# Kernel tuning notes

Measured on AMD Instinct MI355X. Metric: run time of the kernel, lower is better.

## Reference

```python
import jax, jax.numpy as jnp
import numpy as np

N_ATOMS = 50000
N_EDGES = 1_600_000
N_MOL = 500
HIDDEN = 128
FILTERS = 128
GAUSS = 50
LAYERS = 3
CUTOFF = 10.0
LOG2 = 0.6931471805599453


def ssp(x):
    # ShiftedSoftplus: softplus(x) - log(2)
    return jax.nn.softplus(x) - LOG2


def setup_inputs() -> dict:
    key = jax.random.key(0)
    ks = jax.random.split(key, 24)
    z = jax.random.randint(ks[0], (N_ATOMS,), 0, 100)
    pos = jax.random.uniform(ks[1], (N_ATOMS, 3), jnp.float32) * 5.0  # box keeps d < cutoff
    batch = jnp.sort(jax.random.randint(ks[2], (N_ATOMS,), 0, N_MOL))
    row = jax.random.randint(ks[3], (N_EDGES,), 0, N_ATOMS)
    off = jax.random.randint(ks[4], (N_EDGES,), 1, N_ATOMS)
    col = (row + off) % N_ATOMS  # guarantees row != col (no zero distances)
    edge_index = jnp.stack([row, col])
    def lin(k, fi, fo):
        return jax.random.normal(k, (fi, fo), jnp.float32) * (1.0 / np.sqrt(fi))
    emb = jax.random.normal(ks[5], (100, HIDDEN), jnp.float32)
    mlp1_w = jnp.stack([lin(jax.random.fold_in(ks[6], i), GAUSS, FILTERS) for i in range(LAYERS)])
    mlp1_b = jnp.zeros((LAYERS, FILTERS), jnp.float32)
    mlp2_w = jnp.stack([lin(jax.random.fold_in(ks[7], i), FILTERS, FILTERS) for i in range(LAYERS)])
    mlp2_b = jnp.zeros((LAYERS, FILTERS), jnp.float32)
    lin1_w = jnp.stack([lin(jax.random.fold_in(ks[8], i), HIDDEN, FILTERS) for i in range(LAYERS)])
    lin2_w = jnp.stack([lin(jax.random.fold_in(ks[9], i), FILTERS, HIDDEN) for i in range(LAYERS)])
    lin2_b = jnp.zeros((LAYERS, HIDDEN), jnp.float32)
    int_w = jnp.stack([lin(jax.random.fold_in(ks[10], i), HIDDEN, HIDDEN) for i in range(LAYERS)])
    int_b = jnp.zeros((LAYERS, HIDDEN), jnp.float32)
    out1_w = lin(ks[11], HIDDEN, HIDDEN // 2)
    out1_b = jnp.zeros((HIDDEN // 2,), jnp.float32)
    out2_w = lin(ks[12], HIDDEN // 2, 1)
    out2_b = jnp.zeros((1,), jnp.float32)
    return {"z": z, "pos": pos, "batch": batch, "edge_index": edge_index,
            "emb": emb, "mlp1_w": mlp1_w, "mlp1_b": mlp1_b, "mlp2_w": mlp2_w, "mlp2_b": mlp2_b,
            "lin1_w": lin1_w, "lin2_w": lin2_w, "lin2_b": lin2_b, "int_w": int_w, "int_b": int_b,
            "out1_w": out1_w, "out1_b": out1_b, "out2_w": out2_w, "out2_b": out2_b}


def reference(z, pos, batch, edge_index, emb, mlp1_w, mlp1_b, mlp2_w, mlp2_b,
              lin1_w, lin2_w, lin2_b, int_w, int_b, out1_w, out1_b, out2_w, out2_b):
    row, col = edge_index[0], edge_index[1]  # source j, target i
    d = jnp.linalg.norm(pos[row] - pos[col], axis=-1)  # [E]
    # GaussianSmearing
    offset = jnp.linspace(0.0, CUTOFF, GAUSS)
    coeff = -0.5 / (offset[1] - offset[0]) ** 2
    rbf = jnp.exp(coeff * (d[:, None] - offset[None, :]) ** 2)  # [E, GAUSS]
    # cosine cutoff
    C = 0.5 * (jnp.cos(d * jnp.pi / CUTOFF) + 1.0)  # [E]
    h = emb[z]  # [N, H]
    for l in range(LAYERS):
        W = ssp(rbf @ mlp1_w[l] + mlp1_b[l]) @ mlp2_w[l] + mlp2_b[l]  # [E, F]
        W = W * C[:, None]
        x = h @ lin1_w[l]                 # [N, F]
        msg = x[row] * W                  # gather from source, per-edge filter
        agg = jax.ops.segment_sum(msg, col, num_segments=N_ATOMS)  # scatter-add to targets
        x = agg @ lin2_w[l] + lin2_b[l]
        x = ssp(x)
        x = x @ int_w[l] + int_b[l]
        h = h + x                         # residual
    h = ssp(h @ out1_w + out1_b)
    h = h @ out2_w + out2_b               # [N, 1] per-atom energy
    out = jax.ops.segment_sum(h[:, 0], batch, num_segments=N_MOL)  # 'add' readout
    return out.reshape(-1)
```

## Files before the change

kernel.cpp:

```cpp
#include <hip/hip_runtime.h>
#include <math.h>

#define HID 128
#define NGAUSS 50
#define TBL 2048
#define TBL2 8192
#define DMAX 8.6605f
#define LDX 136

typedef _Float16 h2 __attribute__((ext_vector_type(2)));
typedef _Float16 h4 __attribute__((ext_vector_type(4)));
typedef _Float16 f16x8 __attribute__((ext_vector_type(8)));
typedef float f32x4 __attribute__((ext_vector_type(4)));

__device__ __forceinline__ float sspf(float x) {
  float ax = fabsf(x);
  return fmaxf(x, 0.0f) + log1pf(expf(-ax)) - 0.69314718055994530942f;
}

__device__ __forceinline__ void fma4(float4& a, float s, const float4& w) {
  a.x = fmaf(s, w.x, a.x);
  a.y = fmaf(s, w.y, a.y);
  a.z = fmaf(s, w.z, a.z);
  a.w = fmaf(s, w.w, a.w);
}

__global__ __launch_bounds__(128) void build_table_k(
    const float* __restrict__ w1, const float* __restrict__ b1,
    const float* __restrict__ w2, const float* __restrict__ b2,
    float* __restrict__ tab) {
  int l = blockIdx.x >> 11;
  int ti = blockIdx.x & (TBL - 1);
  int j = threadIdx.x;
  __shared__ float rbf[NGAUSS];
  __shared__ float v1[HID];
  const float step = DMAX / (float)(TBL - 1);
  float d = ti * step;
  if (j < NGAUSS) {
    const float gstep = 10.0f / 49.0f;
    const float gcoeff = -12.005f;
    float diff = d - j * gstep;
    rbf[j] = expf(gcoeff * diff * diff);
  }
  __syncthreads();
  float s = b1[l * HID + j];
  const float* w1p = w1 + l * NGAUSS * HID + j;
  for (int g = 0; g < NGAUSS; g++) s = fmaf(rbf[g], w1p[g * HID], s);
  v1[j] = sspf(s);
  __syncthreads();
  float s2 = b2[l * HID + j];
  const float* w2p = w2 + l * HID * HID + j;
  for (int k = 0; k < HID; k++) s2 = fmaf(v1[k], w2p[k * HID], s2);
  float C = 0.5f * (cosf(d * 0.3141592653589793f) + 1.0f);
  tab[((size_t)l * TBL + ti) * HID + j] = s2 * C;
}

__global__ __launch_bounds__(256) void upsample_k(
    const float* __restrict__ tab, _Float16* __restrict__ tabh) {
  int idx = blockIdx.x * 256 + threadIdx.x;
  if (idx >= 3 * TBL2 * HID) return;
  int ch = idx & 127;
  int i = (idx >> 7) & (TBL2 - 1);
  int l = idx >> 20;
  float t = (float)i * ((float)(TBL - 1) / (float)(TBL2 - 1));
  int i0 = min((int)t, TBL - 2);
  float f = t - (float)i0;
  const float* base = tab + ((size_t)l * TBL + i0) * HID + ch;
  tabh[idx] = (_Float16)fmaf(f, base[HID] - base[0], base[0]);
}

__global__ __launch_bounds__(256) void wtrans9_k(
    const float* __restrict__ lin1, const float* __restrict__ lin2,
    const float* __restrict__ intw, _Float16* __restrict__ out) {
  int b = blockIdx.x;
  const float* src = (b < 3 ? lin1 : (b < 6 ? lin2 : intw)) + (size_t)(b % 3) * HID * HID;
  _Float16* dst = out + (size_t)b * HID * HID;
  __shared__ _Float16 tile[128 * 130];
  int t = threadIdx.x;
  for (int i = t; i < HID * HID; i += 256) tile[(i >> 7) * 130 + (i & 127)] = (_Float16)src[i];
  __syncthreads();
  for (int i = t; i < HID * HID; i += 256) dst[i] = tile[(i & 127) * 130 + (i >> 7)];
}

__global__ __launch_bounds__(256) void emb_gather_k(
    const int* __restrict__ z, const float* __restrict__ emb,
    float* __restrict__ h, int N) {
  int i4 = blockIdx.x * 256 + threadIdx.x;
  if (i4 >= N * 32) return;
  int a = i4 >> 5;
  ((float4*)h)[i4] = ((const float4*)emb)[z[a] * 32 + (i4 & 31)];
}

__global__ __launch_bounds__(256) void edge_prep_k(
    const int* __restrict__ row, const int* __restrict__ col,
    const float* __restrict__ pos, int* __restrict__ tq,
    int* __restrict__ bcount, int E, int nbuck) {
  __shared__ int hist[1024];
  int t = threadIdx.x;
  int e0 = blockIdx.x * 2048;
  for (int j = t; j < nbuck; j += 256) hist[j] = 0;
  __syncthreads();
#pragma unroll
  for (int u = 0; u < 8; u++) {
    int e = e0 + u * 256 + t;
    if (e < E) {
      int r = row[e], c = col[e];
      float dx = pos[r * 3 + 0] - pos[c * 3 + 0];
      float dy = pos[r * 3 + 1] - pos[c * 3 + 1];
      float dz = pos[r * 3 + 2] - pos[c * 3 + 2];
      float d = sqrtf(dx * dx + dy * dy + dz * dz);
      const float inv2 = (float)(TBL2 - 1) / DMAX;
      int q = (int)(d * inv2 + 0.5f);
      tq[e] = min(q, TBL2 - 1);
      atomicAdd(&hist[c >> 6], 1);
    }
  }
  __syncthreads();
  for (int j = t; j < nbuck; j += 256)
    if (hist[j]) atomicAdd(&bcount[j], hist[j]);
}

__global__ __launch_bounds__(256) void bucket_scan_k(
    const int* __restrict__ bcount, int* __restrict__ bstart,
    int* __restrict__ bcur, int nbuck, int* __restrict__ starts, int N) {
  __shared__ int sh[256];
  int t = threadIdx.x;
  int chunk = (nbuck + 255) / 256;
  int b0 = t * chunk;
  int c[8];
  int s = 0;
  for (int j = 0; j < chunk; j++) {
    int idx = b0 + j;
    int v = (idx < nbuck) ? bcount[idx] : 0;
    c[j] = v;
    s += v;
  }
  sh[t] = s;
  __syncthreads();
  for (int o = 1; o < 256; o <<= 1) {
    int v = (t >= o) ? sh[t - o] : 0;
    __syncthreads();
    sh[t] += v;
    __syncthreads();
  }
  int p = (t == 0) ? 0 : sh[t - 1];
  for (int j = 0; j < chunk; j++) {
    int idx = b0 + j;
    if (idx < nbuck) {
      bstart[idx] = p;
      bcur[idx] = p;
      p += c[j];
    }
  }
  if (t == 255) {
    bstart[nbuck] = p;
    starts[N] = p;
  }
}

__global__ __launch_bounds__(256) void scatterA_k(
    const int* __restrict__ row, const int* __restrict__ col,
    const int* __restrict__ tq, int* __restrict__ bcur,
    unsigned long long* __restrict__ tmp, int E, int nbuck) {
  __shared__ int hist[1024];
  __shared__ int base[1024];
  int t = threadIdx.x;
  int e0 = blockIdx.x * 2048;
  for (int j = t; j < nbuck; j += 256) hist[j] = 0;
  __syncthreads();
  int bkt[8];
  int rnk[8];
  unsigned long long key[8];
#pragma unroll
  for (int u = 0; u < 8; u++) {
    int e = e0 + u * 256 + t;
    bkt[u] = -1;
    if (e < E) {
      int c = col[e];
      unsigned int pay = ((unsigned int)row[e] << 13) | (unsigned int)tq[e];
      key[u] = ((unsigned long long)pay << 6) | (unsigned long long)(c & 63);
      bkt[u] = c >> 6;
      rnk[u] = atomicAdd(&hist[bkt[u]], 1);
    }
  }
  __syncthreads();
  for (int j = t; j < nbuck; j += 256)
    base[j] = hist[j] ? atomicAdd(&bcur[j], hist[j]) : 0;
  __syncthreads();
#pragma unroll
  for (int u = 0; u < 8; u++)
    if (bkt[u] >= 0) tmp[(size_t)base[bkt[u]] + rnk[u]] = key[u];
}

__global__ __launch_bounds__(256) void scatterB_k(
    const unsigned long long* __restrict__ tmp, const int* __restrict__ bstart,
    int* __restrict__ starts, unsigned int* __restrict__ payload, int N) {
  int j = blockIdx.x;
  int t = threadIdx.x;
  __shared__ int cnt[64];
  __shared__ int cur[64];
  int rs = bstart[j], re = bstart[j + 1];
  if (t < 64) cnt[t] = 0;
  __syncthreads();
  for (int e = rs + t; e < re; e += 256)
    atomicAdd(&cnt[(int)(tmp[e] & 63)], 1);
  __syncthreads();
  if (t < 64) {
    int mine = cnt[t];
    int v = mine;
    for (int o = 1; o < 64; o <<= 1) {
      int u = __shfl_up(v, o, 64);
      if (t >= o) v += u;
    }
    int excl = v - mine;
    int c = j * 64 + t;
    if (c < N) starts[c] = rs + excl;
    cur[t] = rs + excl;
  }
  __syncthreads();
  for (int e = rs + t; e < re; e += 256) {
    unsigned long long k = tmp[e];
    int p = atomicAdd(&cur[(int)(k & 63)], 1);
    payload[p] = (unsigned int)(k >> 6);
  }
}

__global__ __launch_bounds__(256) void mfma_lin1_k(
    const float* __restrict__ in, const _Float16* __restrict__ Wt,
    _Float16* __restrict__ x16, int N) {
  __shared__ __align__(16) _Float16 Xs[64 * LDX];
  __shared__ __align__(16) _Float16 Ws[128 * LDX];
  int t = threadIdx.x;
  int a0 = blockIdx.x * 64;
#pragma unroll
  for (int p = 0; p < 8; p++) {
    int fi = t + p * 256;
    int a = fi >> 5, kg = fi & 31;
    float4 v = make_float4(0.f, 0.f, 0.f, 0.f);
    if (a0 + a < N) v = ((const float4*)in)[(size_t)(a0 + a) * 32 + kg];
    h4 o;
    o.x = (_Float16)v.x; o.y = (_Float16)v.y;
    o.z = (_Float16)v.z; o.w = (_Float16)v.w;
    *(h4*)&Xs[a * LDX + kg * 4] = o;
  }
#pragma unroll
  for (int p = 0; p < 8; p++) {
    int si = t + p * 256;
    int n = si >> 4, kg = si & 15;
    *(uint4*)&Ws[n * LDX + kg * 8] = ((const uint4*)Wt)[si];
  }
  __syncthreads();
  int lane = t & 63;
  int w = t >> 6;
  int mrow = lane & 15, quad = lane >> 4;
  f32x4 zero = {0.f, 0.f, 0.f, 0.f};
  f32x4 acc[8];
#pragma unroll
  for (int i = 0; i < 8; i++) acc[i] = zero;
#pragma unroll
  for (int kk = 0; kk < 4; kk++) {
    f16x8 af = *(const f16x8*)&Xs[(w * 16 + mrow) * LDX + kk * 32 + quad * 8];
#pragma unroll
    for (int nt = 0; nt < 8; nt++) {
      f16x8 bf = *(const f16x8*)&Ws[(nt * 16 + mrow) * LDX + kk * 32 + quad * 8];
      acc[nt] = __builtin_amdgcn_mfma_f32_16x16x32_f16(af, bf, acc[nt], 0, 0, 0);
    }
  }
  __syncthreads();
#pragma unroll
  for (int nt = 0; nt < 8; nt++)
#pragma unroll
    for (int r = 0; r < 4; r++)
      Xs[(w * 16 + quad * 4 + r) * LDX + nt * 16 + mrow] = (_Float16)acc[nt][r];
  __syncthreads();
#pragma unroll
  for (int p = 0; p < 4; p++) {
    int ci = t + p * 256;
    int a = ci >> 4, kg = ci & 15;
    if (a0 + a < N)
      ((uint4*)x16)[(size_t)(a0 + a) * 16 + kg] = *(uint4*)&Xs[a * LDX + kg * 8];
  }
}

__global__ __launch_bounds__(256) void mfma_fused23_k(
    const _Float16* __restrict__ agg16, const _Float16* __restrict__ W2t,
    const float* __restrict__ b2, const _Float16* __restrict__ W3t,
    const float* __restrict__ b3, float* __restrict__ h, int N) {
  __shared__ __align__(16) _Float16 Xs[64 * LDX];
  __shared__ __align__(16) _Float16 Ws[128 * LDX];
  int t = threadIdx.x;
  int a0 = blockIdx.x * 64;
#pragma unroll
  for (int p = 0; p < 4; p++) {
    int ci = t + p * 256;
    int a = ci >> 4, kg = ci & 15;
    uint4 v = make_uint4(0, 0, 0, 0);
    if (a0 + a < N) v = ((const uint4*)agg16)[(size_t)(a0 + a) * 16 + kg];
    *(uint4*)&Xs[a * LDX + kg * 8] = v;
  }
#pragma unroll
  for (int p = 0; p < 8; p++) {
    int si = t + p * 256;
    int n = si >> 4, kg = si & 15;
    *(uint4*)&Ws[n * LDX + kg * 8] = ((const uint4*)W2t)[si];
  }
  __syncthreads();
  int lane = t & 63;
  int w = t >> 6;
  int mrow = lane & 15, quad = lane >> 4;
  f32x4 zero = {0.f, 0.f, 0.f, 0.f};
  f32x4 acc[8];
#pragma unroll
  for (int i = 0; i < 8; i++) acc[i] = zero;
#pragma unroll
  for (int kk = 0; kk < 4; kk++) {
    f16x8 af = *(const f16x8*)&Xs[(w * 16 + mrow) * LDX + kk * 32 + quad * 8];
#pragma unroll
    for (int nt = 0; nt < 8; nt++) {
      f16x8 bf = *(const f16x8*)&Ws[(nt * 16 + mrow) * LDX + kk * 32 + quad * 8];
      acc[nt] = __builtin_amdgcn_mfma_f32_16x16x32_f16(af, bf, acc[nt], 0, 0, 0);
    }
  }
  float b2r[8];
#pragma unroll
  for (int nt = 0; nt < 8; nt++) b2r[nt] = b2[nt * 16 + mrow];
  __syncthreads();
#pragma unroll
  for (int nt = 0; nt < 8; nt++)
#pragma unroll
    for (int r = 0; r < 4; r++)
      Xs[(w * 16 + quad * 4 + r) * LDX + nt * 16 + mrow] = (_Float16)sspf(acc[nt][r] + b2r[nt]);
#pragma unroll
  for (int p = 0; p < 8; p++) {
    int si = t + p * 256;
    int n = si >> 4, kg = si & 15;
    *(uint4*)&Ws[n * LDX + kg * 8] = ((const uint4*)W3t)[si];
  }
  __syncthreads();
#pragma unroll
  for (int i = 0; i < 8; i++) acc[i] = zero;
#pragma unroll
  for (int kk = 0; kk < 4; kk++) {
    f16x8 af = *(const f16x8*)&Xs[(w * 16 + mrow) * LDX + kk * 32 + quad * 8];
#pragma unroll
    for (int nt = 0; nt < 8; nt++) {
      f16x8 bf = *(const f16x8*)&Ws[(nt * 16 + mrow) * LDX + kk * 32 + quad * 8];
      acc[nt] = __builtin_amdgcn_mfma_f32_16x16x32_f16(af, bf, acc[nt], 0, 0, 0);
    }
  }
  float b3r[8];
#pragma unroll
  for (int nt = 0; nt < 8; nt++) b3r[nt] = b3[nt * 16 + mrow];
#pragma unroll
  for (int nt = 0; nt < 8; nt++)
#pragma unroll
    for (int r = 0; r < 4; r++) {
      int a = a0 + w * 16 + quad * 4 + r;
      if (a < N) {
        size_t idx = (size_t)a * HID + nt * 16 + mrow;
        h[idx] += acc[nt][r] + b3r[nt];
      }
    }
}

__global__ __launch_bounds__(256) void aggregate_k(
    const int* __restrict__ starts, const unsigned int* __restrict__ payload,
    const _Float16* __restrict__ x16, const _Float16* __restrict__ tabh,
    _Float16* __restrict__ agg16, int N) {
  int a = blockIdx.x * 4 + (threadIdx.x >> 6);
  if (a >= N) return;
  int lane = threadIdx.x & 63;
  int half = lane >> 5;
  int sl = lane & 31;
  int s = starts[a], e_end = starts[a + 1];
  float4 acc0 = make_float4(0.f, 0.f, 0.f, 0.f);
  float4 acc1 = make_float4(0.f, 0.f, 0.f, 0.f);
  auto do_edge = [&](unsigned int p, float4& acc) {
    int tq = (int)(p & 8191u);
    int r = (int)(p >> 13);
    h4 tw = *(const h4*)&tabh[(size_t)tq * HID + sl * 4];
    h4 xr = *(const h4*)&x16[(size_t)r * HID + sl * 4];
    acc.x = fmaf((float)xr.x, (float)tw.x, acc.x);
    acc.y = fmaf((float)xr.y, (float)tw.y, acc.y);
    acc.z = fmaf((float)xr.z, (float)tw.z, acc.z);
    acc.w = fmaf((float)xr.w, (float)tw.w, acc.w);
  };
  int i = s;
  for (; i + 8 <= e_end; i += 8) {
    unsigned int p0 = payload[i + half];
    unsigned int p1 = payload[i + 2 + half];
    unsigned int p2 = payload[i + 4 + half];
    unsigned int p3 = payload[i + 6 + half];
    do_edge(p0, acc0);
    do_edge(p1, acc1);
    do_edge(p2, acc0);
    do_edge(p3, acc1);
  }
  for (; i < e_end; i += 2) {
    int e = i + half;
    if (e < e_end) do_edge(payload[e], acc0);
  }
  acc0.x += acc1.x; acc0.y += acc1.y; acc0.z += acc1.z; acc0.w += acc1.w;
  acc0.x += __shfl_xor(acc0.x, 32);
  acc0.y += __shfl_xor(acc0.y, 32);
  acc0.z += __shfl_xor(acc0.z, 32);
  acc0.w += __shfl_xor(acc0.w, 32);
  if (half == 0) {
    h4 o;
    o.x = (_Float16)acc0.x; o.y = (_Float16)acc0.y;
    o.z = (_Float16)acc0.z; o.w = (_Float16)acc0.w;
    *(h4*)&agg16[(size_t)a * HID + sl * 4] = o;
  }
}

__global__ __launch_bounds__(256) void atom_energy_k(
    const float* __restrict__ h, const float* __restrict__ o1w,
    const float* __restrict__ o1b, const float* __restrict__ o2w,
    float* __restrict__ e, int N) {
  __shared__ float xs[64 * HID];
  int t = threadIdx.x;
  int a0 = blockIdx.x * 64;
#pragma unroll
  for (int p = 0; p < 8; p++) {
    int fi = t + p * 256;
    int a = a0 + (fi >> 5);
    float4 v = make_float4(0.f, 0.f, 0.f, 0.f);
    if (a < N) v = ((const float4*)h)[(size_t)a * 32 + (fi & 31)];
    ((float4*)xs)[fi] = v;
  }
  __syncthreads();
  int jg = t & 15;
  int ar = t >> 4;
  float4 acc[4];
#pragma unroll
  for (int i = 0; i < 4; i++) acc[i] = make_float4(0.f, 0.f, 0.f, 0.f);
  const float4* Wv = (const float4*)o1w;
  for (int k = 0; k < HID; k += 4) {
    float4 w0 = Wv[(k + 0) * 16 + jg];
    float4 w1 = Wv[(k + 1) * 16 + jg];
    float4 w2 = Wv[(k + 2) * 16 + jg];
    float4 w3 = Wv[(k + 3) * 16 + jg];
#pragma unroll
    for (int i = 0; i < 4; i++) {
      float4 xv = *(const float4*)&xs[(ar * 4 + i) * HID + k];
      float4 a4 = acc[i];
      fma4(a4, xv.x, w0);
      fma4(a4, xv.y, w1);
      fma4(a4, xv.z, w2);
      fma4(a4, xv.w, w3);
      acc[i] = a4;
    }
  }
  float4 b = ((const float4*)o1b)[jg];
  float4 ow = ((const float4*)o2w)[jg];
#pragma unroll
  for (int i = 0; i < 4; i++) {
    float4 v = acc[i];
    float y = sspf(v.x + b.x) * ow.x + sspf(v.y + b.y) * ow.y +
              sspf(v.z + b.z) * ow.z + sspf(v.w + b.w) * ow.w;
    y += __shfl_xor(y, 1);
    y += __shfl_xor(y, 2);
    y += __shfl_xor(y, 4);
    y += __shfl_xor(y, 8);
    int a = a0 + ar * 4 + i;
    if (jg == 0 && a < N) e[a] = y;
  }
}

__global__ __launch_bounds__(256) void seg_sum_k(
    const float* __restrict__ e, const int* __restrict__ batch,
    const float* __restrict__ o2b, float* __restrict__ out, int N) {
  int a = blockIdx.x * 256 + threadIdx.x;
  if (a >= N) return;
  atomicAdd(&out[batch[a]], e[a] + o2b[0]);
}

extern "C" void kernel_launch(void* const* d_in, const int* in_sizes, int n_in,
                              void* d_out, int out_size, void* d_ws, size_t ws_size,
                              hipStream_t stream) {
  const int* z = (const int*)d_in[0];
  const float* pos = (const float*)d_in[1];
  const int* batch = (const int*)d_in[2];
  const int* eidx = (const int*)d_in[3];
  const float* emb = (const float*)d_in[4];
  const float* mlp1_w = (const float*)d_in[5];
  const float* mlp1_b = (const float*)d_in[6];
  const float* mlp2_w = (const float*)d_in[7];
  const float* mlp2_b = (const float*)d_in[8];
  const float* lin1_w = (const float*)d_in[9];
  const float* lin2_w = (const float*)d_in[10];
  const float* lin2_b = (const float*)d_in[11];
  const float* int_w = (const float*)d_in[12];
  const float* int_b = (const float*)d_in[13];
  const float* out1_w = (const float*)d_in[14];
  const float* out1_b = (const float*)d_in[15];
  const float* out2_w = (const float*)d_in[16];
  const float* out2_b = (const float*)d_in[17];
  float* out = (float*)d_out;

  const int N = in_sizes[0];
  const int E = in_sizes[3] / 2;
  const int* row = eidx;
  const int* col = eidx + E;
  const int nbuck = (N + 63) / 64;

  char* ws = (char*)d_ws;
  size_t off = 0;
  auto alloc = [&](size_t bytes) -> void* {
    void* p = ws + off;
    off = (off + bytes + 255) & ~(size_t)255;
    return p;
  };
  float* h = (float*)alloc((size_t)N * HID * 4);
  _Float16* x16 = (_Float16*)alloc((size_t)N * HID * 2);
  size_t agg_bytes = (size_t)N * HID * 2;
  size_t tmp_bytes = (size_t)E * 8 + 16;
  void* agg_union = alloc(agg_bytes > tmp_bytes ? agg_bytes : tmp_bytes);
  _Float16* agg16 = (_Float16*)agg_union;
  unsigned long long* tmp = (unsigned long long*)agg_union;
  int* tq = (int*)alloc((size_t)E * 4);
  unsigned int* payload = (unsigned int*)alloc((size_t)E * 4 + 16);
  int* starts = (int*)alloc((size_t)(N + 1) * 4);
  int* bcount = (int*)alloc((size_t)nbuck * 4);
  int* bstart = (int*)alloc((size_t)(nbuck + 1) * 4);
  int* bcur = (int*)alloc((size_t)nbuck * 4);
  float* tab = (float*)alloc((size_t)3 * TBL * HID * 4);
  _Float16* tabh = (_Float16*)alloc((size_t)3 * TBL2 * HID * 2);
  _Float16* Wt9 = (_Float16*)alloc((size_t)9 * HID * HID * 2);
  float* e_atom = (float*)alloc((size_t)N * 4);
  (void)ws_size;

  hipMemsetAsync(bcount, 0, (size_t)nbuck * 4, stream);
  hipMemsetAsync(out, 0, (size_t)out_size * 4, stream);

  build_table_k<<<3 * TBL, 128, 0, stream>>>(mlp1_w, mlp1_b, mlp2_w, mlp2_b, tab);
  upsample_k<<<(3 * TBL2 * HID + 255) / 256, 256, 0, stream>>>(tab, tabh);
  wtrans9_k<<<9, 256, 0, stream>>>(lin1_w, lin2_w, int_w, Wt9);
  emb_gather_k<<<(N * 32 + 255) / 256, 256, 0, stream>>>(z, emb, h, N);
  edge_prep_k<<<(E + 2047) / 2048, 256, 0, stream>>>(row, col, pos, tq, bcount, E, nbuck);
  bucket_scan_k<<<1, 256, 0, stream>>>(bcount, bstart, bcur, nbuck, starts, N);
  scatterA_k<<<(E + 2047) / 2048, 256, 0, stream>>>(row, col, tq, bcur, tmp, E, nbuck);
  scatterB_k<<<nbuck, 256, 0, stream>>>(tmp, bstart, starts, payload, N);

  int gemm_grid = (N + 63) / 64;
  for (int l = 0; l < 3; l++) {
    const _Float16* W1t = Wt9 + (size_t)l * HID * HID;
    const _Float16* W2t = Wt9 + (size_t)(3 + l) * HID * HID;
    const _Float16* W3t = Wt9 + (size_t)(6 + l) * HID * HID;
    mfma_lin1_k<<<gemm_grid, 256, 0, stream>>>(h, W1t, x16, N);
    aggregate_k<<<(N + 3) / 4, 256, 0, stream>>>(starts, payload, x16,
                                                 tabh + (size_t)l * TBL2 * HID, agg16, N);
    mfma_fused23_k<<<gemm_grid, 256, 0, stream>>>(agg16, W2t, lin2_b + (size_t)l * HID,
                                                  W3t, int_b + (size_t)l * HID, h, N);
  }
  atom_energy_k<<<gemm_grid, 256, 0, stream>>>(h, out1_w, out1_b, out2_w, e_atom, N);
  seg_sum_k<<<(N + 255) / 256, 256, 0, stream>>>(e_atom, batch, out2_b, out, N);
}
```

Measured before the change: 638.2 us.

## Fuse embedding, next-layer lin1, and readout into GEMM kernels; compute distances in scatter

```diff
diff --git a/kernel.cpp b/kernel.cpp
--- a/kernel.cpp
+++ b/kernel.cpp
@@ -16,13 +16,6 @@
 __device__ __forceinline__ float sspf(float x) {
   float ax = fabsf(x);
   return fmaxf(x, 0.0f) + log1pf(expf(-ax)) - 0.69314718055994530942f;
-}
-
-__device__ __forceinline__ void fma4(float4& a, float s, const float4& w) {
-  a.x = fmaf(s, w.x, a.x);
-  a.y = fmaf(s, w.y, a.y);
-  a.z = fmaf(s, w.z, a.z);
-  a.w = fmaf(s, w.w, a.w);
 }
 
 __global__ __launch_bounds__(128) void build_table_k(
@@ -69,32 +62,29 @@
   tabh[idx] = (_Float16)fmaf(f, base[HID] - base[0], base[0]);
 }
 
-__global__ __launch_bounds__(256) void wtrans9_k(
+__global__ __launch_bounds__(256) void wtrans10_k(
     const float* __restrict__ lin1, const float* __restrict__ lin2,
-    const float* __restrict__ intw, _Float16* __restrict__ out) {
+    const float* __restrict__ intw, const float* __restrict__ out1w,
+    _Float16* __restrict__ out) {
   int b = blockIdx.x;
-  const float* src = (b < 3 ? lin1 : (b < 6 ? lin2 : intw)) + (size_t)(b % 3) * HID * HID;
-  _Float16* dst = out + (size_t)b * HID * HID;
   __shared__ _Float16 tile[128 * 130];
   int t = threadIdx.x;
-  for (int i = t; i < HID * HID; i += 256) tile[(i >> 7) * 130 + (i & 127)] = (_Float16)src[i];
-  __syncthreads();
-  for (int i = t; i < HID * HID; i += 256) dst[i] = tile[(i & 127) * 130 + (i >> 7)];
-}
-
-__global__ __launch_bounds__(256) void emb_gather_k(
-    const int* __restrict__ z, const float* __restrict__ emb,
-    float* __restrict__ h, int N) {
-  int i4 = blockIdx.x * 256 + threadIdx.x;
-  if (i4 >= N * 32) return;
-  int a = i4 >> 5;
-  ((float4*)h)[i4] = ((const float4*)emb)[z[a] * 32 + (i4 & 31)];
-}
-
-__global__ __launch_bounds__(256) void edge_prep_k(
-    const int* __restrict__ row, const int* __restrict__ col,
-    const float* __restrict__ pos, int* __restrict__ tq,
-    int* __restrict__ bcount, int E, int nbuck) {
+  if (b < 9) {
+    const float* src = (b < 3 ? lin1 : (b < 6 ? lin2 : intw)) + (size_t)(b % 3) * HID * HID;
+    _Float16* dst = out + (size_t)b * HID * HID;
+    for (int i = t; i < HID * HID; i += 256) tile[(i >> 7) * 130 + (i & 127)] = (_Float16)src[i];
+    __syncthreads();
+    for (int i = t; i < HID * HID; i += 256) dst[i] = tile[(i & 127) * 130 + (i >> 7)];
+  } else {
+    _Float16* dst = out + (size_t)9 * HID * HID;
+    for (int i = t; i < 128 * 64; i += 256) tile[(i >> 6) * 66 + (i & 63)] = (_Float16)out1w[i];
+    __syncthreads();
+    for (int i = t; i < 64 * 128; i += 256) dst[i] = tile[(i & 127) * 66 + (i >> 7)];
+  }
+}
+
+__global__ __launch_bounds__(256) void bcount_k(
+    const int* __restrict__ col, int* __restrict__ bcount, int E, int nbuck) {
   __shared__ int hist[1024];
   int t = threadIdx.x;
   int e0 = blockIdx.x * 2048;
@@ -103,17 +93,7 @@
 #pragma unroll
   for (int u = 0; u < 8; u++) {
     int e = e0 + u * 256 + t;
-    if (e < E) {
-      int r = row[e], c = col[e];
-      float dx = pos[r * 3 + 0] - pos[c * 3 + 0];
-      float dy = pos[r * 3 + 1] - pos[c * 3 + 1];
-      float dz = pos[r * 3 + 2] - pos[c * 3 + 2];
-      float d = sqrtf(dx * dx + dy * dy + dz * dz);
-      const float inv2 = (float)(TBL2 - 1) / DMAX;
-      int q = (int)(d * inv2 + 0.5f);
-      tq[e] = min(q, TBL2 - 1);
-      atomicAdd(&hist[c >> 6], 1);
-    }
+    if (e < E) atomicAdd(&hist[col[e] >> 6], 1);
   }
   __syncthreads();
   for (int j = t; j < nbuck; j += 256)
@@ -160,7 +140,7 @@
 
 __global__ __launch_bounds__(256) void scatterA_k(
     const int* __restrict__ row, const int* __restrict__ col,
-    const int* __restrict__ tq, int* __restrict__ bcur,
+    const float* __restrict__ pos, int* __restrict__ bcur,
     unsigned long long* __restrict__ tmp, int E, int nbuck) {
   __shared__ int hist[1024];
   __shared__ int base[1024];
@@ -176,8 +156,14 @@
     int e = e0 + u * 256 + t;
     bkt[u] = -1;
     if (e < E) {
-      int c = col[e];
-      unsigned int pay = ((unsigned int)row[e] << 13) | (unsigned int)tq[e];
+      int r = row[e], c = col[e];
+      float dx = pos[r * 3 + 0] - pos[c * 3 + 0];
+      float dy = pos[r * 3 + 1] - pos[c * 3 + 1];
+      float dz = pos[r * 3 + 2] - pos[c * 3 + 2];
+      float d = sqrtf(dx * dx + dy * dy + dz * dz);
+      const float inv2 = (float)(TBL2 - 1) / DMAX;
+      int q = min((int)(d * inv2 + 0.5f), TBL2 - 1);
+      unsigned int pay = ((unsigned int)r << 13) | (unsigned int)q;
       key[u] = ((unsigned long long)pay << 6) | (unsigned long long)(c & 63);
       bkt[u] = c >> 6;
       rnk[u] = atomicAdd(&hist[bkt[u]], 1);
@@ -225,19 +211,26 @@
   }
 }
 
-__global__ __launch_bounds__(256) void mfma_lin1_k(
-    const float* __restrict__ in, const _Float16* __restrict__ Wt,
+__global__ __launch_bounds__(256) void lin1_emb_k(
+    const int* __restrict__ z, const float* __restrict__ emb,
+    const _Float16* __restrict__ W1t, float* __restrict__ h,
     _Float16* __restrict__ x16, int N) {
   __shared__ __align__(16) _Float16 Xs[64 * LDX];
   __shared__ __align__(16) _Float16 Ws[128 * LDX];
+  __shared__ int zi[64];
   int t = threadIdx.x;
   int a0 = blockIdx.x * 64;
+  if (t < 64) zi[t] = (a0 + t < N) ? z[a0 + t] : 0;
+  __syncthreads();
 #pragma unroll
   for (int p = 0; p < 8; p++) {
     int fi = t + p * 256;
     int a = fi >> 5, kg = fi & 31;
     float4 v = make_float4(0.f, 0.f, 0.f, 0.f);
-    if (a0 + a < N) v = ((const float4*)in)[(size_t)(a0 + a) * 32 + kg];
+    if (a0 + a < N) {
+      v = ((const float4*)emb)[(size_t)zi[a] * 32 + kg];
+      ((float4*)h)[(size_t)(a0 + a) * 32 + kg] = v;
+    }
     h4 o;
     o.x = (_Float16)v.x; o.y = (_Float16)v.y;
     o.z = (_Float16)v.z; o.w = (_Float16)v.w;
@@ -247,7 +240,7 @@
   for (int p = 0; p < 8; p++) {
     int si = t + p * 256;
     int n = si >> 4, kg = si & 15;
-    *(uint4*)&Ws[n * LDX + kg * 8] = ((const uint4*)Wt)[si];
+    *(uint4*)&Ws[n * LDX + kg * 8] = ((const uint4*)W1t)[si];
   }
   __syncthreads();
   int lane = t & 63;
@@ -282,12 +275,14 @@
   }
 }
 
-__global__ __launch_bounds__(256) void mfma_fused23_k(
+__global__ __launch_bounds__(256) void fused_mid_k(
     const _Float16* __restrict__ agg16, const _Float16* __restrict__ W2t,
     const float* __restrict__ b2, const _Float16* __restrict__ W3t,
-    const float* __restrict__ b3, float* __restrict__ h, int N) {
+    const float* __restrict__ b3, float* __restrict__ h,
+    const _Float16* __restrict__ W1nt, _Float16* __restrict__ x16, int N) {
   __shared__ __align__(16) _Float16 Xs[64 * LDX];
   __shared__ __align__(16) _Float16 Ws[128 * LDX];
+  float* Fs = (float*)Ws;
   int t = threadIdx.x;
   int a0 = blockIdx.x * 64;
 #pragma unroll
@@ -351,16 +346,194 @@
   float b3r[8];
 #pragma unroll
   for (int nt = 0; nt < 8; nt++) b3r[nt] = b3[nt * 16 + mrow];
+  __syncthreads();
 #pragma unroll
   for (int nt = 0; nt < 8; nt++)
 #pragma unroll
-    for (int r = 0; r < 4; r++) {
-      int a = a0 + w * 16 + quad * 4 + r;
-      if (a < N) {
-        size_t idx = (size_t)a * HID + nt * 16 + mrow;
-        h[idx] += acc[nt][r] + b3r[nt];
-      }
-    }
+    for (int r = 0; r < 4; r++)
+      Fs[(w * 16 + quad * 4 + r) * 132 + nt * 16 + mrow] = acc[nt][r] + b3r[nt];
+  __syncthreads();
+#pragma unroll
+  for (int p = 0; p < 8; p++) {
+    int ci = t + p * 256;
+    int a = ci >> 5, kg = ci & 31;
+    float4 v = *(float4*)&Fs[a * 132 + kg * 4];
+    if (a0 + a < N) {
+      float4 ho = ((const float4*)h)[(size_t)(a0 + a) * 32 + kg];
+      v.x += ho.x; v.y += ho.y; v.z += ho.z; v.w += ho.w;
+      ((float4*)h)[(size_t)(a0 + a) * 32 + kg] = v;
+    }
+    h4 o;
+    o.x = (_Float16)v.x; o.y = (_Float16)v.y;
+    o.z = (_Float16)v.z; o.w = (_Float16)v.w;
+    *(h4*)&Xs[a * LDX + kg * 4] = o;
+  }
+  __syncthreads();
+#pragma unroll
+  for (int p = 0; p < 8; p++) {
+    int si = t + p * 256;
+    int n = si >> 4, kg = si & 15;
+    *(uint4*)&Ws[n * LDX + kg * 8] = ((const uint4*)W1nt)[si];
+  }
+  __syncthreads();
+#pragma unroll
+  for (int i = 0; i < 8; i++) acc[i] = zero;
+#pragma unroll
+  for (int kk = 0; kk < 4; kk++) {
+    f16x8 af = *(const f16x8*)&Xs[(w * 16 + mrow) * LDX + kk * 32 + quad * 8];
+#pragma unroll
+    for (int nt = 0; nt < 8; nt++) {
+      f16x8 bf = *(const f16x8*)&Ws[(nt * 16 + mrow) * LDX + kk * 32 + quad * 8];
+      acc[nt] = __builtin_amdgcn_mfma_f32_16x16x32_f16(af, bf, acc[nt], 0, 0, 0);
+    }
+  }
+  __syncthreads();
+#pragma unroll
+  for (int nt = 0; nt < 8; nt++)
+#pragma unroll
+    for (int r = 0; r < 4; r++)
+      Xs[(w * 16 + quad * 4 + r) * LDX + nt * 16 + mrow] = (_Float16)acc[nt][r];
+  __syncthreads();
+#pragma unroll
+  for (int p = 0; p < 4; p++) {
+    int ci = t + p * 256;
+    int a = ci >> 4, kg = ci & 15;
+    if (a0 + a < N)
+      ((uint4*)x16)[(size_t)(a0 + a) * 16 + kg] = *(uint4*)&Xs[a * LDX + kg * 8];
+  }
+}
+
+__global__ __launch_bounds__(256) void fused_last_k(
+    const _Float16* __restrict__ agg16, const _Float16* __restrict__ W2t,
+    const float* __restrict__ b2, const _Float16* __restrict__ W3t,
+    const float* __restrict__ b3, const float* __restrict__ h,
+    const _Float16* __restrict__ Wo1t, const float* __restrict__ o1b,
+    const float* __restrict__ o2w, const float* __restrict__ o2b,
+    const int* __restrict__ batch, float* __restrict__ out, int N) {
+  __shared__ __align__(16) _Float16 Xs[64 * LDX];
+  __shared__ __align__(16) _Float16 Ws[128 * LDX];
+  float* Fs = (float*)Ws;
+  int t = threadIdx.x;
+  int a0 = blockIdx.x * 64;
+#pragma unroll
+  for (int p = 0; p < 4; p++) {
+    int ci = t + p * 256;
+    int a = ci >> 4, kg = ci & 15;
+    uint4 v = make_uint4(0, 0, 0, 0);
+    if (a0 + a < N) v = ((const uint4*)agg16)[(size_t)(a0 + a) * 16 + kg];
+    *(uint4*)&Xs[a * LDX + kg * 8] = v;
+  }
+#pragma unroll
+  for (int p = 0; p < 8; p++) {
+    int si = t + p * 256;
+    int n = si >> 4, kg = si & 15;
+    *(uint4*)&Ws[n * LDX + kg * 8] = ((const uint4*)W2t)[si];
+  }
+  __syncthreads();
+  int lane = t & 63;
+  int w = t >> 6;
+  int mrow = lane & 15, quad = lane >> 4;
+  f32x4 zero = {0.f, 0.f, 0.f, 0.f};
+  f32x4 acc[8];
+#pragma unroll
+  for (int i = 0; i < 8; i++) acc[i] = zero;
+#pragma unroll
+  for (int kk = 0; kk < 4; kk++) {
+    f16x8 af = *(const f16x8*)&Xs[(w * 16 + mrow) * LDX + kk * 32 + quad * 8];
+#pragma unroll
+    for (int nt = 0; nt < 8; nt++) {
+      f16x8 bf = *(const f16x8*)&Ws[(nt * 16 + mrow) * LDX + kk * 32 + quad * 8];
+      acc[nt] = __builtin_amdgcn_mfma_f32_16x16x32_f16(af, bf, acc[nt], 0, 0, 0);
+    }
+  }
+  float b2r[8];
+#pragma unroll
+  for (int nt = 0; nt < 8; nt++) b2r[nt] = b2[nt * 16 + mrow];
+  __syncthreads();
+#pragma unroll
+  for (int nt = 0; nt < 8; nt++)
+#pragma unroll
+    for (int r = 0; r < 4; r++)
+      Xs[(w * 16 + quad * 4 + r) * LDX + nt * 16 + mrow] = (_Float16)sspf(acc[nt][r] + b2r[nt]);
+#pragma unroll
+  for (int p = 0; p < 8; p++) {
+    int si = t + p * 256;
+    int n = si >> 4, kg = si & 15;
+    *(uint4*)&Ws[n * LDX + kg * 8] = ((const uint4*)W3t)[si];
+  }
+  __syncthreads();
+#pragma unroll
+  for (int i = 0; i < 8; i++) acc[i] = zero;
+#pragma unroll
+  for (int kk = 0; kk < 4; kk++) {
+    f16x8 af = *(const f16x8*)&Xs[(w * 16 + mrow) * LDX + kk * 32 + quad * 8];
+#pragma unroll
+    for (int nt = 0; nt < 8; nt++) {
+      f16x8 bf = *(const f16x8*)&Ws[(nt * 16 + mrow) * LDX + kk * 32 + quad * 8];
+      acc[nt] = __builtin_amdgcn_mfma_f32_16x16x32_f16(af, bf, acc[nt], 0, 0, 0);
+    }
+  }
+  float b3r[8];
+#pragma unroll
+  for (int nt = 0; nt < 8; nt++) b3r[nt] = b3[nt * 16 + mrow];
+  __syncthreads();
+#pragma unroll
+  for (int nt = 0; nt < 8; nt++)
+#pragma unroll
+    for (int r = 0; r < 4; r++)
+      Fs[(w * 16 + quad * 4 + r) * 132 + nt * 16 + mrow] = acc[nt][r] + b3r[nt];
+  __syncthreads();
+#pragma unroll
+  for (int p = 0; p < 8; p++) {
+    int ci = t + p * 256;
+    int a = ci >> 5, kg = ci & 31;
+    float4 v = *(float4*)&Fs[a * 132 + kg * 4];
+    if (a0 + a < N) {
+      float4 ho = ((const float4*)h)[(size_t)(a0 + a) * 32 + kg];
+      v.x += ho.x; v.y += ho.y; v.z += ho.z; v.w += ho.w;
+    }
+    h4 o;
+    o.x = (_Float16)v.x; o.y = (_Float16)v.y;
+    o.z = (_Float16)v.z; o.w = (_Float16)v.w;
+    *(h4*)&Xs[a * LDX + kg * 4] = o;
+  }
+  __syncthreads();
+#pragma unroll
+  for (int p = 0; p < 4; p++) {
+    int si = t + p * 256;
+    int n = si >> 4, kg = si & 15;
+    *(uint4*)&Ws[n * LDX + kg * 8] = ((const uint4*)Wo1t)[si];
+  }
+  __syncthreads();
+#pragma unroll
+  for (int i = 0; i < 4; i++) acc[i] = zero;
+#pragma unroll
+  for (int kk = 0; kk < 4; kk++) {
+    f16x8 af = *(const f16x8*)&Xs[(w * 16 + mrow) * LDX + kk * 32 + quad * 8];
+#pragma unroll
+    for (int nt = 0; nt < 4; nt++) {
+      f16x8 bf = *(const f16x8*)&Ws[(nt * 16 + mrow) * LDX + kk * 32 + quad * 8];
+      acc[nt] = __builtin_amdgcn_mfma_f32_16x16x32_f16(af, bf, acc[nt], 0, 0, 0);
+    }
+  }
+  float o2b0 = o2b[0];
+  float ss[4] = {0.f, 0.f, 0.f, 0.f};
+#pragma unroll
+  for (int nt = 0; nt < 4; nt++) {
+    float bb = o1b[nt * 16 + mrow];
+    float ww = o2w[nt * 16 + mrow];
+#pragma unroll
+    for (int r = 0; r < 4; r++) ss[r] += sspf(acc[nt][r] + bb) * ww;
+  }
+#pragma unroll
+  for (int r = 0; r < 4; r++) {
+    ss[r] += __shfl_xor(ss[r], 1);
+    ss[r] += __shfl_xor(ss[r], 2);
+    ss[r] += __shfl_xor(ss[r], 4);
+    ss[r] += __shfl_xor(ss[r], 8);
+    int a = a0 + w * 16 + quad * 4 + r;
+    if (mrow == 0 && a < N) atomicAdd(&out[batch[a]], ss[r] + o2b0);
+  }
 }
 
 __global__ __launch_bounds__(256) void aggregate_k(
@@ -413,68 +586,6 @@
   }
 }
 
-__global__ __launch_bounds__(256) void atom_energy_k(
-    const float* __restrict__ h, const float* __restrict__ o1w,
-    const float* __restrict__ o1b, const float* __restrict__ o2w,
-    float* __restrict__ e, int N) {
-  __shared__ float xs[64 * HID];
-  int t = threadIdx.x;
-  int a0 = blockIdx.x * 64;
-#pragma unroll
-  for (int p = 0; p < 8; p++) {
-    int fi = t + p * 256;
-    int a = a0 + (fi >> 5);
-    float4 v = make_float4(0.f, 0.f, 0.f, 0.f);
-    if (a < N) v = ((const float4*)h)[(size_t)a * 32 + (fi & 31)];
-    ((float4*)xs)[fi] = v;
-  }
-  __syncthreads();
-  int jg = t & 15;
-  int ar = t >> 4;
-  float4 acc[4];
-#pragma unroll
-  for (int i = 0; i < 4; i++) acc[i] = make_float4(0.f, 0.f, 0.f, 0.f);
-  const float4* Wv = (const float4*)o1w;
-  for (int k = 0; k < HID; k += 4) {
-    float4 w0 = Wv[(k + 0) * 16 + jg];
-    float4 w1 = Wv[(k + 1) * 16 + jg];
-    float4 w2 = Wv[(k + 2) * 16 + jg];
-    float4 w3 = Wv[(k + 3) * 16 + jg];
-#pragma unroll
-    for (int i = 0; i < 4; i++) {
-      float4 xv = *(const float4*)&xs[(ar * 4 + i) * HID + k];
-      float4 a4 = acc[i];
-      fma4(a4, xv.x, w0);
-      fma4(a4, xv.y, w1);
-      fma4(a4, xv.z, w2);
-      fma4(a4, xv.w, w3);
-      acc[i] = a4;
-    }
-  }
-  float4 b = ((const float4*)o1b)[jg];
-  float4 ow = ((const float4*)o2w)[jg];
-#pragma unroll
-  for (int i = 0; i < 4; i++) {
-    float4 v = acc[i];
-    float y = sspf(v.x + b.x) * ow.x + sspf(v.y + b.y) * ow.y +
-              sspf(v.z + b.z) * ow.z + sspf(v.w + b.w) * ow.w;
-    y += __shfl_xor(y, 1);
-    y += __shfl_xor(y, 2);
-    y += __shfl_xor(y, 4);
-    y += __shfl_xor(y, 8);
-    int a = a0 + ar * 4 + i;
-    if (jg == 0 && a < N) e[a] = y;
-  }
-}
-
-__global__ __launch_bounds__(256) void seg_sum_k(
-    const float* __restrict__ e, const int* __restrict__ batch,
-    const float* __restrict__ o2b, float* __restrict__ out, int N) {
-  int a = blockIdx.x * 256 + threadIdx.x;
-  if (a >= N) return;
-  atomicAdd(&out[batch[a]], e[a] + o2b[0]);
-}
-
 extern "C" void kernel_launch(void* const* d_in, const int* in_sizes, int n_in,
                               void* d_out, int out_size, void* d_ws, size_t ws_size,
                               hipStream_t stream) {
@@ -518,7 +629,6 @@
   void* agg_union = alloc(agg_bytes > tmp_bytes ? agg_bytes : tmp_bytes);
   _Float16* agg16 = (_Float16*)agg_union;
   unsigned long long* tmp = (unsigned long long*)agg_union;
-  int* tq = (int*)alloc((size_t)E * 4);
   unsigned int* payload = (unsigned int*)alloc((size_t)E * 4 + 16);
   int* starts = (int*)alloc((size_t)(N + 1) * 4);
   int* bcount = (int*)alloc((size_t)nbuck * 4);
@@ -526,8 +636,7 @@
   int* bcur = (int*)alloc((size_t)nbuck * 4);
   float* tab = (float*)alloc((size_t)3 * TBL * HID * 4);
   _Float16* tabh = (_Float16*)alloc((size_t)3 * TBL2 * HID * 2);
-  _Float16* Wt9 = (_Float16*)alloc((size_t)9 * HID * HID * 2);
-  float* e_atom = (float*)alloc((size_t)N * 4);
+  _Float16* Wt10 = (_Float16*)alloc((size_t)10 * HID * HID * 2);
   (void)ws_size;
 
   hipMemsetAsync(bcount, 0, (size_t)nbuck * 4, stream);
@@ -535,24 +644,26 @@
 
   build_table_k<<<3 * TBL, 128, 0, stream>>>(mlp1_w, mlp1_b, mlp2_w, mlp2_b, tab);
   upsample_k<<<(3 * TBL2 * HID + 255) / 256, 256, 0, stream>>>(tab, tabh);
-  wtrans9_k<<<9, 256, 0, stream>>>(lin1_w, lin2_w, int_w, Wt9);
-  emb_gather_k<<<(N * 32 + 255) / 256, 256, 0, stream>>>(z, emb, h, N);
-  edge_prep_k<<<(E + 2047) / 2048, 256, 0, stream>>>(row, col, pos, tq, bcount, E, nbuck);
+  wtrans10_k<<<10, 256, 0, stream>>>(lin1_w, lin2_w, int_w, out1_w, Wt10);
+  bcount_k<<<(E + 2047) / 2048, 256, 0, stream>>>(col, bcount, E, nbuck);
   bucket_scan_k<<<1, 256, 0, stream>>>(bcount, bstart, bcur, nbuck, starts, N);
-  scatterA_k<<<(E + 2047) / 2048, 256, 0, stream>>>(row, col, tq, bcur, tmp, E, nbuck);
+  scatterA_k<<<(E + 2047) / 2048, 256, 0, stream>>>(row, col, pos, bcur, tmp, E, nbuck);
   scatterB_k<<<nbuck, 256, 0, stream>>>(tmp, bstart, starts, payload, N);
 
   int gemm_grid = (N + 63) / 64;
-  for (int l = 0; l < 3; l++) {
-    const _Float16* W1t = Wt9 + (size_t)l * HID * HID;
-    const _Float16* W2t = Wt9 + (size_t)(3 + l) * HID * HID;
-    const _Float16* W3t = Wt9 + (size_t)(6 + l) * HID * HID;
-    mfma_lin1_k<<<gemm_grid, 256, 0, stream>>>(h, W1t, x16, N);
+  lin1_emb_k<<<gemm_grid, 256, 0, stream>>>(z, emb, Wt10, h, x16, N);
+  for (int l = 0; l < 2; l++) {
     aggregate_k<<<(N + 3) / 4, 256, 0, stream>>>(starts, payload, x16,
                                                  tabh + (size_t)l * TBL2 * HID, agg16, N);
-    mfma_fused23_k<<<gemm_grid, 256, 0, stream>>>(agg16, W2t, lin2_b + (size_t)l * HID,
-                                                  W3t, int_b + (size_t)l * HID, h, N);
-  }
-  atom_energy_k<<<gemm_grid, 256, 0, stream>>>(h, out1_w, out1_b, out2_w, e_atom, N);
-  seg_sum_k<<<(N + 255) / 256, 256, 0, stream>>>(e_atom, batch, out2_b, out, N);
-}
+    fused_mid_k<<<gemm_grid, 256, 0, stream>>>(
+        agg16, Wt10 + (size_t)(3 + l) * HID * HID, lin2_b + (size_t)l * HID,
+        Wt10 + (size_t)(6 + l) * HID * HID, int_b + (size_t)l * HID, h,
+        Wt10 + (size_t)(l + 1) * HID * HID, x16, N);
+  }
+  aggregate_k<<<(N + 3) / 4, 256, 0, stream>>>(starts, payload, x16,
+                                               tabh + (size_t)2 * TBL2 * HID, agg16, N);
+  fused_last_k<<<gemm_grid, 256, 0, stream>>>(
+      agg16, Wt10 + (size_t)5 * HID * HID, lin2_b + (size_t)2 * HID,
+      Wt10 + (size_t)8 * HID * HID, int_b + (size_t)2 * HID, h,
+      Wt10 + (size_t)9 * HID * HID, out1_b, out2_w, out2_b, batch, out, N);
+}
```

New measurement: 586.8 us. 1.09x faster.
